# Optimization experiments

Measured on AMD Instinct MI355X. Metric: run time of the kernel, lower is better.

The kernel has to match this reference:

```python
import jax, jax.numpy as jnp
import numpy as np

NUM_NODES = 100000
NUM_REL = 8
HIDDEN = 128
NUM_EDGES = 1600000
NUM_LAYERS = 2


def setup_inputs() -> dict:
    key = jax.random.key(0)
    k1, k2, k3, k4, k5 = jax.random.split(key, 5)
    x = jnp.arange(NUM_NODES, dtype=jnp.int64)
    edge_index = jax.random.randint(k1, (2, NUM_EDGES), 0, NUM_NODES, dtype=jnp.int64)
    edge_type = jax.random.randint(k2, (NUM_EDGES,), 0, NUM_REL, dtype=jnp.int64)
    emb = jax.random.normal(k3, (NUM_NODES, HIDDEN), dtype=jnp.float32) * 0.1
    W = jax.random.normal(k4, (NUM_LAYERS, NUM_REL, HIDDEN, HIDDEN), dtype=jnp.float32) * (1.0 / np.sqrt(HIDDEN))
    root = jax.random.normal(k5, (NUM_LAYERS, HIDDEN, HIDDEN), dtype=jnp.float32) * (1.0 / np.sqrt(HIDDEN))
    bias = jnp.zeros((NUM_LAYERS, HIDDEN), dtype=jnp.float32)
    return {"x": x, "edge_index": edge_index, "edge_type": edge_type,
            "emb": emb, "W": W, "root": root, "bias": bias}


def _rgcn_conv(h, src, dst, etype, W_l, root_l, bias_l):
    # h: [N, d]; W_l: [R, d, d]
    n = h.shape[0]
    r = W_l.shape[0]
    # Transform all nodes by every relation weight: [R, N, d]
    xW = jnp.einsum('nd,rdf->rnf', h, W_l)
    # Per-edge message gathered by (relation, source): [E, d]
    msg = xW[etype, src]
    # Mean-normalize per (target node, relation), matching PyG aggr='mean'
    seg = dst * r + etype  # combined (node, relation) segment id
    cnt = jax.ops.segment_sum(jnp.ones(msg.shape[0], dtype=h.dtype), seg,
                              num_segments=n * r)
    norm = 1.0 / jnp.maximum(cnt[seg], 1.0)
    agg = jax.ops.segment_sum(msg * norm[:, None], dst, num_segments=n)
    return agg + h @ root_l + bias_l


def reference(x, edge_index, edge_type, emb, W, root, bias):
    src, dst = edge_index[0], edge_index[1]
    h = emb[x]  # embedding lookup
    for l in range(NUM_LAYERS):
        h = _rgcn_conv(h, src, dst, edge_type, W[l], root[l], bias[l])
        h = jax.nn.relu(h)
    return h
```

## Files before the change

kernel.cpp:

```cpp
#include <hip/hip_runtime.h>

typedef unsigned int u32;
typedef unsigned short u16;
typedef __attribute__((ext_vector_type(8))) short short8;
typedef __attribute__((ext_vector_type(4))) float f32x4;

#define DD 128
#define RREL 8
#define AMW 1024
#define NKT 9
#define SCAN_CHUNK 4096

static __device__ __forceinline__ u16 f2bf(float f) {
  u32 u = __builtin_bit_cast(u32, f);
  u32 r = (u + 0x7fffu + ((u >> 16) & 1u)) >> 16;
  return (u16)r;
}
static __device__ __forceinline__ float bflo(u32 v) { return __builtin_bit_cast(float, v << 16); }
static __device__ __forceinline__ float bfhi(u32 v) { return __builtin_bit_cast(float, v & 0xffff0000u); }

__global__ __launch_bounds__(256) void k_convw(const float* __restrict__ W,
                                               const float* __restrict__ root,
                                               uint4* __restrict__ wt) {
  int t = blockIdx.x * 256 + threadIdx.x;
  if (t >= 2 * NKT * 2048) return;
  int l = t / (NKT * 2048);
  int rem = t - l * (NKT * 2048);
  int kt = rem >> 11;
  int pos = rem & 2047;
  int col = pos >> 4;
  int cbx = pos & 15;
  int cb = cbx ^ (col & 7);
  int k0 = kt * DD + cb * 8;
  u16 vals[8];
#pragma unroll
  for (int i = 0; i < 8; ++i) {
    int k = k0 + i;
    float v;
    if (k < DD) {
      v = root[(size_t)l * DD * DD + k * DD + col];
    } else {
      int km = k - DD;
      v = W[((size_t)l * RREL + (km >> 7)) * DD * DD + (size_t)(km & 127) * DD + col];
    }
    vals[i] = f2bf(v);
  }
  wt[t] = *(uint4*)vals;
}

__global__ __launch_bounds__(256) void k_gather(const int* __restrict__ x,
                                                const float* __restrict__ emb,
                                                u16* __restrict__ h0, int N) {
  int t = blockIdx.x * 256 + threadIdx.x;
  if (t >= N * 16) return;
  int node = t >> 4, part = t & 15;
  const float4* e4 = (const float4*)(emb + (size_t)x[node] * DD + part * 8);
  float4 f0 = e4[0], f1 = e4[1];
  uint4 u;
  u.x = (u32)f2bf(f0.x) | ((u32)f2bf(f0.y) << 16);
  u.y = (u32)f2bf(f0.z) | ((u32)f2bf(f0.w) << 16);
  u.z = (u32)f2bf(f1.x) | ((u32)f2bf(f1.y) << 16);
  u.w = (u32)f2bf(f1.z) | ((u32)f2bf(f1.w) << 16);
  *(uint4*)(h0 + (size_t)node * DD + part * 8) = u;
}

__global__ __launch_bounds__(256) void k_hist(const int* __restrict__ ei,
                                              const int* __restrict__ et,
                                              int* __restrict__ cnt, int E) {
  int base = (blockIdx.x * 256 + threadIdx.x) * 4;
  if (base + 3 < E) {
    int4 d4 = *(const int4*)(ei + E + base);
    int4 t4 = *(const int4*)(et + base);
    atomicAdd(&cnt[d4.x * 8 + t4.x], 1);
    atomicAdd(&cnt[d4.y * 8 + t4.y], 1);
    atomicAdd(&cnt[d4.z * 8 + t4.z], 1);
    atomicAdd(&cnt[d4.w * 8 + t4.w], 1);
  } else {
    for (int e = base; e < E; ++e) atomicAdd(&cnt[ei[E + e] * 8 + et[e]], 1);
  }
}

__global__ __launch_bounds__(256) void k_scan_reduce(const int* __restrict__ cnt,
                                                     int* __restrict__ blksum, int nseg) {
  __shared__ int s[256];
  int b = blockIdx.x, t = threadIdx.x;
  int base = b * SCAN_CHUNK;
  int sum = 0;
  for (int i = 0; i < 16; ++i) {
    int idx = base + i * 256 + t;
    if (idx < nseg) sum += cnt[idx];
  }
  s[t] = sum;
  __syncthreads();
  for (int st = 128; st > 0; st >>= 1) {
    if (t < st) s[t] += s[t + st];
    __syncthreads();
  }
  if (t == 0) blksum[b] = s[0];
}

__global__ void k_scan_top(int* __restrict__ blksum, int nblk, int* __restrict__ off,
                           int nseg, int E) {
  if (threadIdx.x == 0 && blockIdx.x == 0) {
    int run = 0;
    for (int b = 0; b < nblk; ++b) { int v = blksum[b]; blksum[b] = run; run += v; }
    off[nseg] = E;
  }
}

__global__ __launch_bounds__(256) void k_scan_write(const int* __restrict__ cnt,
                                                    const int* __restrict__ blksum,
                                                    int* __restrict__ off,
                                                    int* __restrict__ fill, int nseg) {
  __shared__ int s[256];
  int b = blockIdx.x, t = threadIdx.x;
  int base = b * SCAN_CHUNK + t * 16;
  int v[16];
  int sum = 0;
#pragma unroll
  for (int i = 0; i < 16; ++i) {
    int idx = base + i;
    v[i] = (idx < nseg) ? cnt[idx] : 0;
    sum += v[i];
  }
  s[t] = sum;
  __syncthreads();
  for (int st = 1; st < 256; st <<= 1) {
    int add = (t >= st) ? s[t - st] : 0;
    __syncthreads();
    s[t] += add;
    __syncthreads();
  }
  int run = blksum[b] + s[t] - sum;
#pragma unroll
  for (int i = 0; i < 16; ++i) {
    int idx = base + i;
    if (idx < nseg) { off[idx] = run; fill[idx] = run; }
    run += v[i];
  }
}

__global__ __launch_bounds__(256) void k_scatter(const int* __restrict__ ei,
                                                 const int* __restrict__ et,
                                                 int* __restrict__ fill,
                                                 int* __restrict__ sorted, int E) {
  int base = (blockIdx.x * 256 + threadIdx.x) * 4;
  if (base + 3 < E) {
    int4 s4 = *(const int4*)(ei + base);
    int4 d4 = *(const int4*)(ei + E + base);
    int4 t4 = *(const int4*)(et + base);
    int p0 = atomicAdd(&fill[d4.x * 8 + t4.x], 1);
    int p1 = atomicAdd(&fill[d4.y * 8 + t4.y], 1);
    int p2 = atomicAdd(&fill[d4.z * 8 + t4.z], 1);
    int p3 = atomicAdd(&fill[d4.w * 8 + t4.w], 1);
    sorted[p0] = s4.x;
    sorted[p1] = s4.y;
    sorted[p2] = s4.z;
    sorted[p3] = s4.w;
  } else {
    for (int e = base; e < E; ++e) {
      int pos = atomicAdd(&fill[ei[E + e] * 8 + et[e]], 1);
      sorted[pos] = ei[e];
    }
  }
}

static __device__ __forceinline__ void add8(float* a, uint4 v) {
  a[0] += bflo(v.x); a[1] += bfhi(v.x);
  a[2] += bflo(v.y); a[3] += bfhi(v.y);
  a[4] += bflo(v.z); a[5] += bfhi(v.z);
  a[6] += bflo(v.w); a[7] += bfhi(v.w);
}

__global__ __launch_bounds__(256) void k_agg(const int* __restrict__ off,
                                             const int* __restrict__ sorted,
                                             const u16* __restrict__ hin,
                                             u16* __restrict__ am, int N, int E) {
  int wave = threadIdx.x >> 6, lane = threadIdx.x & 63;
  int grp = lane >> 3, oct = lane & 7;
  int dst = blockIdx.x * 32 + wave * 8 + grp;
  if (dst >= N) return;
  int4 b0 = *(const int4*)(off + dst * 8);
  int4 b1 = *(const int4*)(off + dst * 8 + 4);
  int je = off[dst * 8 + 8];
  int cs = b0.x;
  int e1 = b0.y, e2 = b0.z, e3 = b0.w, e4 = b1.x, e5 = b1.y, e6 = b1.z, e7 = b1.w, e8 = je;
  u16* ambase = am + (size_t)dst * AMW + oct * 16;
  float a[16];
#pragma unroll
  for (int i = 0; i < 16; ++i) a[i] = 0.f;
  int j = cs;
  int r = 0;
  int lastidx = (E > 0) ? E - 1 : 0;
  while (true) {
    while (r < 8 && j >= e1) {
      int cnt = e1 - cs;
      float norm = (cnt > 0) ? 1.0f / (float)cnt : 0.f;
      uint4 w0, w1;
      w0.x = (u32)f2bf(a[0] * norm) | ((u32)f2bf(a[1] * norm) << 16);
      w0.y = (u32)f2bf(a[2] * norm) | ((u32)f2bf(a[3] * norm) << 16);
      w0.z = (u32)f2bf(a[4] * norm) | ((u32)f2bf(a[5] * norm) << 16);
      w0.w = (u32)f2bf(a[6] * norm) | ((u32)f2bf(a[7] * norm) << 16);
      w1.x = (u32)f2bf(a[8] * norm) | ((u32)f2bf(a[9] * norm) << 16);
      w1.y = (u32)f2bf(a[10] * norm) | ((u32)f2bf(a[11] * norm) << 16);
      w1.z = (u32)f2bf(a[12] * norm) | ((u32)f2bf(a[13] * norm) << 16);
      w1.w = (u32)f2bf(a[14] * norm) | ((u32)f2bf(a[15] * norm) << 16);
      uint4* outp = (uint4*)(ambase + (size_t)r * DD);
      outp[0] = w0;
      outp[1] = w1;
#pragma unroll
      for (int i = 0; i < 16; ++i) a[i] = 0.f;
      cs = e1;
      e1 = e2; e2 = e3; e3 = e4; e4 = e5; e5 = e6; e6 = e7; e7 = e8;
      ++r;
    }
    if (r >= 8) break;
    int j1 = j + 1;
    bool two = (j1 < e1);
    int s0 = sorted[j];
    int s1 = sorted[two ? j1 : lastidx];
    const uint4* p0 = (const uint4*)(hin + (size_t)s0 * DD + oct * 16);
    const uint4* p1 = (const uint4*)(hin + (size_t)s1 * DD + oct * 16);
    uint4 v0 = p0[0], v0b = p0[1];
    uint4 v1 = p1[0], v1b = p1[1];
    if (!two) {
      v1.x = v1.y = v1.z = v1.w = 0u;
      v1b.x = v1b.y = v1b.z = v1b.w = 0u;
    }
    add8(a, v0); add8(a + 8, v0b);
    add8(a, v1); add8(a + 8, v1b);
    j += two ? 2 : 1;
  }
}

template <bool LAST>
__global__ __launch_bounds__(512) void k_gemm(const u16* __restrict__ h,
                                              const u16* __restrict__ am,
                                              const uint4* __restrict__ wt,
                                              const float* __restrict__ bias,
                                              u16* __restrict__ hout,
                                              float* __restrict__ dout, int M) {
  __shared__ uint4 ldsB[2][2048];
  int tid = threadIdx.x, wave = tid >> 6, lane = tid & 63;
  int rowbase = blockIdx.x * 128 + wave * 16;
  int arow = rowbase + (lane & 15);
  int arc = arow < M ? arow : M - 1;
  int klane = (lane >> 4) << 3;
  f32x4 acc[8];
#pragma unroll
  for (int c = 0; c < 8; ++c) acc[c] = (f32x4)0.f;

#define STAGE(KT, BUF)                                                                   \
  do {                                                                                   \
    const uint4* gsrc = wt + (size_t)(KT) * 2048;                                        \
    _Pragma("unroll") for (int i_ = 0; i_ < 4; ++i_) {                                   \
      int cid_ = i_ * 512 + tid;                                                         \
      __builtin_amdgcn_global_load_lds(                                                  \
          (const __attribute__((address_space(1))) uint4*)(gsrc + cid_),                 \
          (__attribute__((address_space(3))) uint4*)&ldsB[BUF][cid_], 16, 0, 0);         \
    }                                                                                    \
  } while (0)

  STAGE(0, 0);
  for (int kt = 0; kt < NKT; ++kt) {
    int cur = kt & 1;
    __syncthreads();
    if (kt + 1 < NKT) STAGE(kt + 1, cur ^ 1);
    const u16* abase = (kt == 0) ? (h + (size_t)arc * DD)
                                 : (am + (size_t)arc * AMW + (kt - 1) * DD);
#pragma unroll
    for (int kc = 0; kc < 4; ++kc) {
      short8 a = *(const short8*)(abase + kc * 32 + klane);
      int chunk = kc * 4 + (lane >> 4);
#pragma unroll
      for (int c = 0; c < 8; ++c) {
        int col = c * 16 + (lane & 15);
        const short8* bp = (const short8*)&ldsB[cur][col * 16 + (chunk ^ (col & 7))];
        acc[c] = __builtin_amdgcn_mfma_f32_16x16x32_bf16(a, *bp, acc[c], 0, 0, 0);
      }
    }
  }
#undef STAGE

  int crow0 = rowbase + ((lane >> 4) << 2);
  int ccol = lane & 15;
#pragma unroll
  for (int c = 0; c < 8; ++c) {
    int col = c * 16 + ccol;
    float bv = bias[col];
#pragma unroll
    for (int i = 0; i < 4; ++i) {
      int row = crow0 + i;
      if (row < M) {
        float v = fmaxf(acc[c][i] + bv, 0.f);
        if (LAST) dout[(size_t)row * DD + col] = v;
        else hout[(size_t)row * DD + col] = f2bf(v);
      }
    }
  }
}

extern "C" void kernel_launch(void* const* d_in, const int* in_sizes, int n_in,
                              void* d_out, int out_size, void* d_ws, size_t ws_size,
                              hipStream_t stream) {
  const int* x = (const int*)d_in[0];
  const int* ei = (const int*)d_in[1];
  const int* et = (const int*)d_in[2];
  const float* emb = (const float*)d_in[3];
  const float* W = (const float*)d_in[4];
  const float* root = (const float*)d_in[5];
  const float* bias = (const float*)d_in[6];

  const int N = in_sizes[0];
  const int E = in_sizes[2];
  const int NSEG = N * RREL;

  size_t o = 0;
  auto al = [&](size_t b) { size_t r = o; o = (o + b + 255) & ~(size_t)255; return r; };
  size_t off_o = al(((size_t)NSEG + 1) * 4);
  size_t cnt_o = al((size_t)NSEG * 4);
  size_t fill_o = al((size_t)NSEG * 4);
  size_t sorted_o = al((size_t)E * 4);
  size_t blk_o = al(4096);
  size_t wt_o = al((size_t)2 * NKT * 2048 * 16);
  size_t h0_o = al((size_t)N * DD * 2);
  size_t am_o = al((size_t)N * AMW * 2);
  (void)am_o;

  char* ws = (char*)d_ws;
  int* off = (int*)(ws + off_o);
  int* cnt = (int*)(ws + cnt_o);
  int* fill = (int*)(ws + fill_o);
  int* sorted = (int*)(ws + sorted_o);
  int* blks = (int*)(ws + blk_o);
  uint4* wt = (uint4*)(ws + wt_o);
  u16* h0 = (u16*)(ws + h0_o);
  u16* am = (u16*)(ws + am_o);
  float* outf = (float*)d_out;

  k_convw<<<(2 * NKT * 2048 + 255) / 256, 256, 0, stream>>>(W, root, wt);
  k_gather<<<(N * 16 + 255) / 256, 256, 0, stream>>>(x, emb, h0, N);
  hipMemsetAsync(cnt, 0, (size_t)NSEG * 4, stream);
  k_hist<<<((E + 3) / 4 + 255) / 256, 256, 0, stream>>>(ei, et, cnt, E);
  int nblk = (NSEG + SCAN_CHUNK - 1) / SCAN_CHUNK;
  k_scan_reduce<<<nblk, 256, 0, stream>>>(cnt, blks, NSEG);
  k_scan_top<<<1, 64, 0, stream>>>(blks, nblk, off, NSEG, E);
  k_scan_write<<<nblk, 256, 0, stream>>>(cnt, blks, off, fill, NSEG);
  k_scatter<<<((E + 3) / 4 + 255) / 256, 256, 0, stream>>>(ei, et, fill, sorted, E);

  int gx = (N + 127) / 128;
  int agrid = (N + 31) / 32;
  k_agg<<<agrid, 256, 0, stream>>>(off, sorted, h0, am, N, E);
  k_gemm<false><<<gx, 512, 0, stream>>>(h0, am, wt, bias, h0, nullptr, N);
  k_agg<<<agrid, 256, 0, stream>>>(off, sorted, h0, am, N, E);
  k_gemm<true><<<gx, 512, 0, stream>>>(h0, am, wt + (size_t)NKT * 2048, bias + DD,
                                       nullptr, outf, N);
}
```

Measured before the change: 568.9 us.

## Chunk aggregation and GEMM over node ranges to keep aggregate buffer cache-resident

Splits each layer's aggregate-then-GEMM over node chunks of 25000, so the per-relation aggregate buffer is a reusable chunk-sized buffer instead of a full N x 1024 bf16 array. The aim is for the intermediate to stay in the large last-level cache between k_agg and k_gemm rather than spilling to HBM. It also adds a separate h1 buffer, because the layer-0 GEMM can no longer overwrite h0 in place when a later chunk still reads it. The histogram and scatter kernels are simplified to one edge per thread, dropping the int4 vectorised loads. The chunking adds more kernel launches and smaller grids per launch.

```diff
diff --git a/kernel.cpp b/kernel.cpp
--- a/kernel.cpp
+++ b/kernel.cpp
@@ -10,6 +10,7 @@
 #define AMW 1024
 #define NKT 9
 #define SCAN_CHUNK 4096
+#define NCHUNK 25000
 
 static __device__ __forceinline__ u16 f2bf(float f) {
   u32 u = __builtin_bit_cast(u32, f);
@@ -67,17 +68,10 @@
 __global__ __launch_bounds__(256) void k_hist(const int* __restrict__ ei,
                                               const int* __restrict__ et,
                                               int* __restrict__ cnt, int E) {
-  int base = (blockIdx.x * 256 + threadIdx.x) * 4;
-  if (base + 3 < E) {
-    int4 d4 = *(const int4*)(ei + E + base);
-    int4 t4 = *(const int4*)(et + base);
-    atomicAdd(&cnt[d4.x * 8 + t4.x], 1);
-    atomicAdd(&cnt[d4.y * 8 + t4.y], 1);
-    atomicAdd(&cnt[d4.z * 8 + t4.z], 1);
-    atomicAdd(&cnt[d4.w * 8 + t4.w], 1);
-  } else {
-    for (int e = base; e < E; ++e) atomicAdd(&cnt[ei[E + e] * 8 + et[e]], 1);
-  }
+  int e = blockIdx.x * 256 + threadIdx.x;
+  if (e >= E) return;
+  int dst = ei[E + e];
+  atomicAdd(&cnt[dst * 8 + et[e]], 1);
 }
 
 __global__ __launch_bounds__(256) void k_scan_reduce(const int* __restrict__ cnt,
@@ -144,25 +138,11 @@
                                                  const int* __restrict__ et,
                                                  int* __restrict__ fill,
                                                  int* __restrict__ sorted, int E) {
-  int base = (blockIdx.x * 256 + threadIdx.x) * 4;
-  if (base + 3 < E) {
-    int4 s4 = *(const int4*)(ei + base);
-    int4 d4 = *(const int4*)(ei + E + base);
-    int4 t4 = *(const int4*)(et + base);
-    int p0 = atomicAdd(&fill[d4.x * 8 + t4.x], 1);
-    int p1 = atomicAdd(&fill[d4.y * 8 + t4.y], 1);
-    int p2 = atomicAdd(&fill[d4.z * 8 + t4.z], 1);
-    int p3 = atomicAdd(&fill[d4.w * 8 + t4.w], 1);
-    sorted[p0] = s4.x;
-    sorted[p1] = s4.y;
-    sorted[p2] = s4.z;
-    sorted[p3] = s4.w;
-  } else {
-    for (int e = base; e < E; ++e) {
-      int pos = atomicAdd(&fill[ei[E + e] * 8 + et[e]], 1);
-      sorted[pos] = ei[e];
-    }
-  }
+  int e = blockIdx.x * 256 + threadIdx.x;
+  if (e >= E) return;
+  int src = ei[e], dst = ei[E + e];
+  int pos = atomicAdd(&fill[dst * 8 + et[e]], 1);
+  sorted[pos] = src;
 }
 
 static __device__ __forceinline__ void add8(float* a, uint4 v) {
@@ -175,17 +155,18 @@
 __global__ __launch_bounds__(256) void k_agg(const int* __restrict__ off,
                                              const int* __restrict__ sorted,
                                              const u16* __restrict__ hin,
-                                             u16* __restrict__ am, int N, int E) {
+                                             u16* __restrict__ am, int dst0, int dend,
+                                             int E) {
   int wave = threadIdx.x >> 6, lane = threadIdx.x & 63;
   int grp = lane >> 3, oct = lane & 7;
-  int dst = blockIdx.x * 32 + wave * 8 + grp;
-  if (dst >= N) return;
+  int dst = dst0 + blockIdx.x * 32 + wave * 8 + grp;
+  if (dst >= dend) return;
   int4 b0 = *(const int4*)(off + dst * 8);
   int4 b1 = *(const int4*)(off + dst * 8 + 4);
   int je = off[dst * 8 + 8];
   int cs = b0.x;
   int e1 = b0.y, e2 = b0.z, e3 = b0.w, e4 = b1.x, e5 = b1.y, e6 = b1.z, e7 = b1.w, e8 = je;
-  u16* ambase = am + (size_t)dst * AMW + oct * 16;
+  u16* ambase = am + (size_t)(dst - dst0) * AMW + oct * 16;
   float a[16];
 #pragma unroll
   for (int i = 0; i < 16; ++i) a[i] = 0.f;
@@ -239,12 +220,13 @@
                                               const uint4* __restrict__ wt,
                                               const float* __restrict__ bias,
                                               u16* __restrict__ hout,
-                                              float* __restrict__ dout, int M) {
+                                              float* __restrict__ dout, int row0,
+                                              int row1) {
   __shared__ uint4 ldsB[2][2048];
   int tid = threadIdx.x, wave = tid >> 6, lane = tid & 63;
-  int rowbase = blockIdx.x * 128 + wave * 16;
+  int rowbase = row0 + blockIdx.x * 128 + wave * 16;
   int arow = rowbase + (lane & 15);
-  int arc = arow < M ? arow : M - 1;
+  int arc = arow < row1 ? arow : row1 - 1;
   int klane = (lane >> 4) << 3;
   f32x4 acc[8];
 #pragma unroll
@@ -267,7 +249,7 @@
     __syncthreads();
     if (kt + 1 < NKT) STAGE(kt + 1, cur ^ 1);
     const u16* abase = (kt == 0) ? (h + (size_t)arc * DD)
-                                 : (am + (size_t)arc * AMW + (kt - 1) * DD);
+                                 : (am + (size_t)(arc - row0) * AMW + (kt - 1) * DD);
 #pragma unroll
     for (int kc = 0; kc < 4; ++kc) {
       short8 a = *(const short8*)(abase + kc * 32 + klane);
@@ -291,7 +273,7 @@
 #pragma unroll
     for (int i = 0; i < 4; ++i) {
       int row = crow0 + i;
-      if (row < M) {
+      if (row < row1) {
         float v = fmaxf(acc[c][i] + bv, 0.f);
         if (LAST) dout[(size_t)row * DD + col] = v;
         else hout[(size_t)row * DD + col] = f2bf(v);
@@ -324,7 +306,8 @@
   size_t blk_o = al(4096);
   size_t wt_o = al((size_t)2 * NKT * 2048 * 16);
   size_t h0_o = al((size_t)N * DD * 2);
-  size_t am_o = al((size_t)N * AMW * 2);
+  size_t h1_o = al((size_t)N * DD * 2);
+  size_t am_o = al((size_t)NCHUNK * AMW * 2);
   (void)am_o;
 
   char* ws = (char*)d_ws;
@@ -335,24 +318,32 @@
   int* blks = (int*)(ws + blk_o);
   uint4* wt = (uint4*)(ws + wt_o);
   u16* h0 = (u16*)(ws + h0_o);
+  u16* h1 = (u16*)(ws + h1_o);
   u16* am = (u16*)(ws + am_o);
   float* outf = (float*)d_out;
 
   k_convw<<<(2 * NKT * 2048 + 255) / 256, 256, 0, stream>>>(W, root, wt);
   k_gather<<<(N * 16 + 255) / 256, 256, 0, stream>>>(x, emb, h0, N);
   hipMemsetAsync(cnt, 0, (size_t)NSEG * 4, stream);
-  k_hist<<<((E + 3) / 4 + 255) / 256, 256, 0, stream>>>(ei, et, cnt, E);
+  k_hist<<<(E + 255) / 256, 256, 0, stream>>>(ei, et, cnt, E);
   int nblk = (NSEG + SCAN_CHUNK - 1) / SCAN_CHUNK;
   k_scan_reduce<<<nblk, 256, 0, stream>>>(cnt, blks, NSEG);
   k_scan_top<<<1, 64, 0, stream>>>(blks, nblk, off, NSEG, E);
   k_scan_write<<<nblk, 256, 0, stream>>>(cnt, blks, off, fill, NSEG);
-  k_scatter<<<((E + 3) / 4 + 255) / 256, 256, 0, stream>>>(ei, et, fill, sorted, E);
-
-  int gx = (N + 127) / 128;
-  int agrid = (N + 31) / 32;
-  k_agg<<<agrid, 256, 0, stream>>>(off, sorted, h0, am, N, E);
-  k_gemm<false><<<gx, 512, 0, stream>>>(h0, am, wt, bias, h0, nullptr, N);
-  k_agg<<<agrid, 256, 0, stream>>>(off, sorted, h0, am, N, E);
-  k_gemm<true><<<gx, 512, 0, stream>>>(h0, am, wt + (size_t)NKT * 2048, bias + DD,
-                                       nullptr, outf, N);
-}
+  k_scatter<<<(E + 255) / 256, 256, 0, stream>>>(ei, et, fill, sorted, E);
+
+  for (int l = 0; l < 2; ++l) {
+    const u16* hin = l ? h1 : h0;
+    for (int c0 = 0; c0 < N; c0 += NCHUNK) {
+      int c1 = c0 + NCHUNK < N ? c0 + NCHUNK : N;
+      int rows = c1 - c0;
+      k_agg<<<(rows + 31) / 32, 256, 0, stream>>>(off, sorted, hin, am, c0, c1, E);
+      int gx = (rows + 127) / 128;
+      if (l == 0)
+        k_gemm<false><<<gx, 512, 0, stream>>>(hin, am, wt, bias, h1, nullptr, c0, c1);
+      else
+        k_gemm<true><<<gx, 512, 0, stream>>>(hin, am, wt + (size_t)NKT * 2048, bias + DD,
+                                             nullptr, outf, c0, c1);
+    }
+  }
+}
```

New measurement: 684.9 us. 20.4% more time.

## Pre-partition edges into 8 destination buckets before histogram and scatter

Applied to the files above, without the earlier changes.

Adds a two-pass bucketing step that splits edges by destination-node range into 8 buckets: a per-block count, a scan, and a stable block-local partition through LDS. The histogram and scatter then run bucket by bucket, so their atomics and writes hit a narrower region of the count, fill and sorted arrays. This is meant to improve cache locality of the random atomics during CSR construction. It costs three extra kernel launches and an extra read/write pass over the edge data, staged in the aggregation buffer.

```diff
diff --git a/kernel.cpp b/kernel.cpp
--- a/kernel.cpp
+++ b/kernel.cpp
@@ -10,6 +10,7 @@
 #define AMW 1024
 #define NKT 9
 #define SCAN_CHUNK 4096
+#define EPB 1024
 
 static __device__ __forceinline__ u16 f2bf(float f) {
   u32 u = __builtin_bit_cast(u32, f);
@@ -64,19 +65,156 @@
   *(uint4*)(h0 + (size_t)node * DD + part * 8) = u;
 }
 
-__global__ __launch_bounds__(256) void k_hist(const int* __restrict__ ei,
+__global__ __launch_bounds__(256) void k_cnt8(const int* __restrict__ eid,
+                                              int* __restrict__ cnt8, int E, int N8,
+                                              int nblk) {
+  __shared__ u32 s[4];
+  int blk = blockIdx.x, tid = threadIdx.x;
+  if (tid < 4) s[tid] = 0;
+  __syncthreads();
+  int e0 = blk * EPB + tid * 4;
+  u32 c0 = 0, c1 = 0, c2 = 0, c3 = 0;
+#pragma unroll
+  for (int i = 0; i < 4; ++i) {
+    int e = e0 + i;
+    if (e < E) {
+      int b = eid[e] / N8;
+      c0 += (u32)(b == 0) + ((u32)(b == 1) << 16);
+      c1 += (u32)(b == 2) + ((u32)(b == 3) << 16);
+      c2 += (u32)(b == 4) + ((u32)(b == 5) << 16);
+      c3 += (u32)(b == 6) + ((u32)(b == 7) << 16);
+    }
+  }
+  atomicAdd(&s[0], c0); atomicAdd(&s[1], c1);
+  atomicAdd(&s[2], c2); atomicAdd(&s[3], c3);
+  __syncthreads();
+  if (tid == 0) {
+#pragma unroll
+    for (int b = 0; b < 8; ++b)
+      cnt8[b * nblk + blk] = (int)((s[b >> 1] >> ((b & 1) * 16)) & 0xffffu);
+  }
+}
+
+__global__ void k_scan8(const int* __restrict__ cnt8, int* __restrict__ bases8, int n,
+                        int E) {
+  __shared__ int s[256];
+  int tid = threadIdx.x;
+  int ch = (n + 255) / 256;
+  int lo = tid * ch, hi = lo + ch < n ? lo + ch : n;
+  int sum = 0;
+  for (int m = lo; m < hi; ++m) sum += cnt8[m];
+  s[tid] = sum;
+  __syncthreads();
+  for (int st = 1; st < 256; st <<= 1) {
+    int add = (tid >= st) ? s[tid - st] : 0;
+    __syncthreads();
+    s[tid] += add;
+    __syncthreads();
+  }
+  int run = tid ? s[tid - 1] : 0;
+  for (int m = lo; m < hi; ++m) {
+    bases8[m] = run;
+    run += cnt8[m];
+  }
+  if (tid == 255) bases8[n] = E;
+}
+
+__global__ __launch_bounds__(256) void k_part(const int* __restrict__ ei,
                                               const int* __restrict__ et,
-                                              int* __restrict__ cnt, int E) {
-  int base = (blockIdx.x * 256 + threadIdx.x) * 4;
-  if (base + 3 < E) {
-    int4 d4 = *(const int4*)(ei + E + base);
-    int4 t4 = *(const int4*)(et + base);
-    atomicAdd(&cnt[d4.x * 8 + t4.x], 1);
-    atomicAdd(&cnt[d4.y * 8 + t4.y], 1);
-    atomicAdd(&cnt[d4.z * 8 + t4.z], 1);
-    atomicAdd(&cnt[d4.w * 8 + t4.w], 1);
-  } else {
-    for (int e = base; e < E; ++e) atomicAdd(&cnt[ei[E + e] * 8 + et[e]], 1);
+                                              const int* __restrict__ bases8,
+                                              int* __restrict__ bsrc,
+                                              int* __restrict__ bseg, int E, int N8,
+                                              int nblk) {
+  __shared__ u32 pscan[256][4];
+  __shared__ int lstart[9];
+  __shared__ u16 pref[256][8];
+  __shared__ int lsrc[EPB];
+  __shared__ int lseg[EPB];
+  int blk = blockIdx.x, tid = threadIdx.x;
+  int base = blk * EPB;
+  int nE = E - base; if (nE > EPB) nE = EPB;
+  int e0 = base + tid * 4;
+  int bk[4], sv[4], gv[4];
+  u32 c0 = 0, c1 = 0, c2 = 0, c3 = 0;
+#pragma unroll
+  for (int i = 0; i < 4; ++i) {
+    int e = e0 + i;
+    if (e < E) {
+      int d = ei[E + e];
+      sv[i] = ei[e];
+      gv[i] = d * 8 + et[e];
+      int b = d / N8;
+      bk[i] = b;
+      c0 += (u32)(b == 0) + ((u32)(b == 1) << 16);
+      c1 += (u32)(b == 2) + ((u32)(b == 3) << 16);
+      c2 += (u32)(b == 4) + ((u32)(b == 5) << 16);
+      c3 += (u32)(b == 6) + ((u32)(b == 7) << 16);
+    } else {
+      bk[i] = -1; sv[i] = 0; gv[i] = 0;
+    }
+  }
+  pscan[tid][0] = c0; pscan[tid][1] = c1; pscan[tid][2] = c2; pscan[tid][3] = c3;
+  __syncthreads();
+  for (int st = 1; st < 256; st <<= 1) {
+    u32 a0 = 0, a1 = 0, a2 = 0, a3 = 0;
+    if (tid >= st) {
+      a0 = pscan[tid - st][0]; a1 = pscan[tid - st][1];
+      a2 = pscan[tid - st][2]; a3 = pscan[tid - st][3];
+    }
+    __syncthreads();
+    pscan[tid][0] += a0; pscan[tid][1] += a1; pscan[tid][2] += a2; pscan[tid][3] += a3;
+    __syncthreads();
+  }
+  u32 p0 = pscan[tid][0] - c0, p1 = pscan[tid][1] - c1;
+  u32 p2 = pscan[tid][2] - c2, p3 = pscan[tid][3] - c3;
+  if (tid == 0) {
+    u32 t0 = pscan[255][0], t1 = pscan[255][1], t2 = pscan[255][2], t3 = pscan[255][3];
+    int run = 0;
+    int tv[8] = {(int)(t0 & 0xffff), (int)(t0 >> 16), (int)(t1 & 0xffff), (int)(t1 >> 16),
+                 (int)(t2 & 0xffff), (int)(t2 >> 16), (int)(t3 & 0xffff), (int)(t3 >> 16)};
+#pragma unroll
+    for (int b = 0; b < 8; ++b) { lstart[b] = run; run += tv[b]; }
+    lstart[8] = run;
+  }
+  __syncthreads();
+  pref[tid][0] = (u16)(lstart[0] + (p0 & 0xffff));
+  pref[tid][1] = (u16)(lstart[1] + (p0 >> 16));
+  pref[tid][2] = (u16)(lstart[2] + (p1 & 0xffff));
+  pref[tid][3] = (u16)(lstart[3] + (p1 >> 16));
+  pref[tid][4] = (u16)(lstart[4] + (p2 & 0xffff));
+  pref[tid][5] = (u16)(lstart[5] + (p2 >> 16));
+  pref[tid][6] = (u16)(lstart[6] + (p3 & 0xffff));
+  pref[tid][7] = (u16)(lstart[7] + (p3 >> 16));
+#pragma unroll
+  for (int i = 0; i < 4; ++i) {
+    if (bk[i] >= 0) {
+      int slot = pref[tid][bk[i]];
+      pref[tid][bk[i]] = (u16)(slot + 1);
+      lsrc[slot] = sv[i];
+      lseg[slot] = gv[i];
+    }
+  }
+  __syncthreads();
+  for (int j = tid; j < nE; j += 256) {
+    int b = 0;
+#pragma unroll
+    for (int k = 1; k < 8; ++k) b += (j >= lstart[k]);
+    int gpos = bases8[b * nblk + blk] + (j - lstart[b]);
+    bsrc[gpos] = lsrc[j];
+    bseg[gpos] = lseg[j];
+  }
+}
+
+__global__ __launch_bounds__(256) void k_histb(const int* __restrict__ bseg,
+                                               const int* __restrict__ bases8,
+                                               int* __restrict__ cnt, int nblk) {
+  int b = blockIdx.x & 7, chunk = blockIdx.x >> 3;
+  int lo = bases8[b * nblk], hi = bases8[(b + 1) * nblk];
+  int idx = lo + chunk * EPB + threadIdx.x * 4;
+#pragma unroll
+  for (int i = 0; i < 4; ++i) {
+    int e = idx + i;
+    if (e < hi) atomicAdd(&cnt[bseg[e]], 1);
   }
 }
 
@@ -140,27 +278,20 @@
   }
 }
 
-__global__ __launch_bounds__(256) void k_scatter(const int* __restrict__ ei,
-                                                 const int* __restrict__ et,
-                                                 int* __restrict__ fill,
-                                                 int* __restrict__ sorted, int E) {
-  int base = (blockIdx.x * 256 + threadIdx.x) * 4;
-  if (base + 3 < E) {
-    int4 s4 = *(const int4*)(ei + base);
-    int4 d4 = *(const int4*)(ei + E + base);
-    int4 t4 = *(const int4*)(et + base);
-    int p0 = atomicAdd(&fill[d4.x * 8 + t4.x], 1);
-    int p1 = atomicAdd(&fill[d4.y * 8 + t4.y], 1);
-    int p2 = atomicAdd(&fill[d4.z * 8 + t4.z], 1);
-    int p3 = atomicAdd(&fill[d4.w * 8 + t4.w], 1);
-    sorted[p0] = s4.x;
-    sorted[p1] = s4.y;
-    sorted[p2] = s4.z;
-    sorted[p3] = s4.w;
-  } else {
-    for (int e = base; e < E; ++e) {
-      int pos = atomicAdd(&fill[ei[E + e] * 8 + et[e]], 1);
-      sorted[pos] = ei[e];
+__global__ __launch_bounds__(256) void k_scatterb(const int* __restrict__ bsrc,
+                                                  const int* __restrict__ bseg,
+                                                  const int* __restrict__ bases8,
+                                                  int* __restrict__ fill,
+                                                  int* __restrict__ sorted, int nblk) {
+  int b = blockIdx.x & 7, chunk = blockIdx.x >> 3;
+  int lo = bases8[b * nblk], hi = bases8[(b + 1) * nblk];
+  int idx = lo + chunk * EPB + threadIdx.x * 4;
+#pragma unroll
+  for (int i = 0; i < 4; ++i) {
+    int e = idx + i;
+    if (e < hi) {
+      int pos = atomicAdd(&fill[bseg[e]], 1);
+      sorted[pos] = bsrc[e];
     }
   }
 }
@@ -314,6 +445,8 @@
   const int N = in_sizes[0];
   const int E = in_sizes[2];
   const int NSEG = N * RREL;
+  const int N8 = (N + 7) / 8;
+  const int nblkE = (E + EPB - 1) / EPB;
 
   size_t o = 0;
   auto al = [&](size_t b) { size_t r = o; o = (o + b + 255) & ~(size_t)255; return r; };
@@ -336,17 +469,24 @@
   uint4* wt = (uint4*)(ws + wt_o);
   u16* h0 = (u16*)(ws + h0_o);
   u16* am = (u16*)(ws + am_o);
+  int* bsrc = (int*)(ws + am_o);
+  int* bseg = bsrc + E;
+  int* cnt8 = bseg + E;
+  int* bases8 = cnt8 + 8 * nblkE;
   float* outf = (float*)d_out;
 
   k_convw<<<(2 * NKT * 2048 + 255) / 256, 256, 0, stream>>>(W, root, wt);
   k_gather<<<(N * 16 + 255) / 256, 256, 0, stream>>>(x, emb, h0, N);
   hipMemsetAsync(cnt, 0, (size_t)NSEG * 4, stream);
-  k_hist<<<((E + 3) / 4 + 255) / 256, 256, 0, stream>>>(ei, et, cnt, E);
+  k_cnt8<<<nblkE, 256, 0, stream>>>(ei + E, cnt8, E, N8, nblkE);
+  k_scan8<<<1, 256, 0, stream>>>(cnt8, bases8, 8 * nblkE, E);
+  k_part<<<nblkE, 256, 0, stream>>>(ei, et, bases8, bsrc, bseg, E, N8, nblkE);
+  k_histb<<<8 * nblkE, 256, 0, stream>>>(bseg, bases8, cnt, nblkE);
   int nblk = (NSEG + SCAN_CHUNK - 1) / SCAN_CHUNK;
   k_scan_reduce<<<nblk, 256, 0, stream>>>(cnt, blks, NSEG);
   k_scan_top<<<1, 64, 0, stream>>>(blks, nblk, off, NSEG, E);
   k_scan_write<<<nblk, 256, 0, stream>>>(cnt, blks, off, fill, NSEG);
-  k_scatter<<<((E + 3) / 4 + 255) / 256, 256, 0, stream>>>(ei, et, fill, sorted, E);
+  k_scatterb<<<8 * nblkE, 256, 0, stream>>>(bsrc, bseg, bases8, fill, sorted, nblkE);
 
   int gx = (N + 127) / 128;
   int agrid = (N + 31) / 32;
```

Measured after the change: 571.2 us. Within noise of the previous version (+0.4%).
